# Kernel optimization log

Hardware: AMD Instinct MI355X
Metric: run time of the kernel (lower is better)

Reference implementation:

```python
import jax, jax.numpy as jnp
import numpy as np

EMB = 512
QKV = 512
H = 8      # num_heads
PH = 8     # num_pheads
HD = QKV // H
PHD = QKV // PH


def _make_params(key):
    names = ['Wi', 'Wip', 'Wic', 'Wq', 'Wpq', 'Wk', 'Wpk', 'Wv', 'Wpv', 'Wo', 'Wop']
    ks = jax.random.split(key, len(names))
    p = {}
    for n, k in zip(names, ks):
        din = EMB if n in ('Wi', 'Wip', 'Wic') else QKV
        dout = EMB if n in ('Wo', 'Wop') else QKV
        p[n] = jax.random.normal(k, (din, dout), jnp.float32) * 0.02
        p['b' + n[1:]] = jnp.zeros((dout,), jnp.float32)
    return p


def setup_inputs() -> dict:
    key = jax.random.key(0)
    kq, kp, kc, kw = jax.random.split(key, 4)
    B, S, P = 16, 4096, 64
    inp = {
        'query': jax.random.normal(kq, (B, S, EMB), jnp.float32),
        'pquery': jax.random.normal(kp, (B, P, EMB), jnp.float32),
        'context': jax.random.normal(kc, (B, S, EMB), jnp.float32),
    }
    inp.update(_make_params(kw))
    return inp


def reference(query, pquery, context,
              Wi, bi, Wip, bip, Wic, bic,
              Wq, bq, Wpq, bpq, Wk, bk, Wpk, bpk,
              Wv, bv, Wpv, bpv, Wo, bo, Wop, bop):
    # Dropout layers act as identity (eval mode / deterministic reference).
    B, S, _ = query.shape
    P = pquery.shape[1]

    q_in = query @ Wi + bi        # (B,S,QKV)
    pq_in = pquery @ Wip + bip    # (B,P,QKV)
    c_in = context @ Wic + bic    # (B,S,QKV)

    # --- pack stage: pquery attends over context -> p_context ---
    pq = ((pq_in @ Wpq + bpq) * (PHD ** -0.5)).reshape(B, P, PH, PHD)
    pk = (c_in @ Wpk + bpk).reshape(B, S, PH, PHD)
    pv = (c_in @ Wpv + bpv).reshape(B, S, PH, PHD)
    # dropout before softmax in original; identity here
    pattn = jax.nn.softmax(jnp.einsum('bphd,bshd->bhps', pq, pk), axis=-1)
    pc = jnp.einsum('bhps,bshd->bphd', pattn, pv).reshape(B, P, QKV)

    # --- unpack stage: query attends over p_context ---
    q = ((q_in @ Wq + bq) * (HD ** -0.5)).reshape(B, S, H, HD)
    k = (pc @ Wk + bk).reshape(B, P, H, HD)
    v = (pc @ Wv + bv).reshape(B, P, H, HD)
    aw = jax.nn.softmax(jnp.einsum('bshd,bphd->bhsp', q, k), axis=-1)  # (B,H,S,P)
    attn = jnp.einsum('bhsp,bphd->bshd', aw, v).reshape(B, S, QKV)
    attn = attn @ Wo + bo           # (B,S,EMB)
    pc_out = pc @ Wop + bop         # (B,P,EMB)

    # torch returns attn_weights as (S, B*H, P) when batch_first
    aw_t = jnp.transpose(aw.reshape(B * H, S, P), (1, 0, 2))
    return attn, pc_out, aw_t
```

## Files before the change

### kernel.cpp

```cpp
#include <hip/hip_runtime.h>


typedef __bf16 bf16x8 __attribute__((ext_vector_type(8)));
typedef float f32x4 __attribute__((ext_vector_type(4)));
typedef unsigned short u16x8 __attribute__((ext_vector_type(8)));
typedef unsigned short u16x4 __attribute__((ext_vector_type(4)));

#define MFMA16(a, b, c) __builtin_amdgcn_mfma_f32_16x16x32_bf16((a), (b), (c), 0, 0, 0)

__device__ __forceinline__ unsigned short f2bf_bits(float f) {
  unsigned int u = __float_as_uint(f);
  u += 0x7fffu + ((u >> 16) & 1u);
  return (unsigned short)(u >> 16);
}

__device__ __forceinline__ void gload16(const void* g, void* l) {
  __builtin_amdgcn_global_load_lds(
      (const __attribute__((address_space(1))) void*)g,
      (__attribute__((address_space(3))) void*)l, 16, 0, 0);
}

struct Ptr8 { const float* p[8]; };

__global__ __launch_bounds__(256) void prep_kernel(
    Ptr8 srcs, unsigned short* __restrict__ WT,
    const float* bi, const float* bip, const float* bic,
    const float* Wq, const float* Wpq, const float* Wpk, const float* Wpv,
    const float* bq, const float* bpq, const float* bpk, const float* bpv,
    float* __restrict__ bias_out) {
  const int t = threadIdx.x;
  if (blockIdx.z < 8) {
    const float* __restrict__ W = srcs.p[blockIdx.z];
    unsigned short* __restrict__ O = WT + (size_t)blockIdx.z * 262144;
    __shared__ float tile[32][33];
    const int tr = blockIdx.x * 32, tc = blockIdx.y * 32;
    {
      const int r = t >> 3, c4 = (t & 7) * 4;
      const float4 v = *reinterpret_cast<const float4*>(&W[(size_t)(tr + r) * 512 + tc + c4]);
      tile[r][c4 + 0] = v.x; tile[r][c4 + 1] = v.y; tile[r][c4 + 2] = v.z; tile[r][c4 + 3] = v.w;
    }
    __syncthreads();
    {
      const int n = t >> 3, k4 = (t & 7) * 4;
      u16x4 o;
#pragma unroll
      for (int j = 0; j < 4; j++) o[j] = f2bf_bits(tile[k4 + j][n]);
      *reinterpret_cast<u16x4*>(&O[(size_t)(tc + n) * 512 + tr + k4]) = o;
    }
  } else {
    const int idx = blockIdx.y * 16 + blockIdx.x;
    if (idx >= 8) return;
    const int y = idx >> 1;
    const float* bin  = (y == 0) ? bi : (y == 1) ? bip : bic;
    const float* W    = (y == 0) ? Wq : (y == 1) ? Wpq : (y == 2) ? Wpk : Wpv;
    const float* bout = (y == 0) ? bq : (y == 1) ? bpq : (y == 2) ? bpk : bpv;
    const float scale = (y < 2) ? 0.125f : 1.0f;
    const int n = (idx & 1) * 256 + t;
    float s = 0.f;
    for (int k = 0; k < 512; k++) s += bin[k] * W[(size_t)k * 512 + n];
    bias_out[y * 512 + n] = (s + bout[n]) * scale;
  }
}

__global__ __launch_bounds__(256) void gemm_wcomb(
    const float* __restrict__ Wi, const float* __restrict__ Wip,
    const float* __restrict__ Wic, const unsigned short* __restrict__ WTbase,
    unsigned short* __restrict__ outbase) {
  const int z = blockIdx.z;
  const float* __restrict__ A = (z == 0) ? Wi : (z == 1) ? Wip : Wic;
  const unsigned short* __restrict__ BT = WTbase + (size_t)z * 262144;
  unsigned short* __restrict__ out = outbase + (size_t)z * 262144;
  const float scale = (z < 2) ? 0.125f : 1.0f;

  __shared__ __align__(16) unsigned short As[128 * 72];
  __shared__ __align__(16) unsigned short Bs[128 * 72];
  const int t = threadIdx.x;
  const int w = t >> 6, l = t & 63, li = l & 15, lg = l >> 4;
  const int wm = w >> 1, wn = w & 1;
  const int m0 = blockIdx.x * 128, n0 = blockIdx.y * 128;

  f32x4 acc[4][4] = {};

  for (int kt = 0; kt < 512; kt += 64) {
#pragma unroll
    for (int i = 0; i < 8; i++) {
      const int row = i * 16 + (t >> 4), k = (t & 15) * 4;
      const float4 v = *reinterpret_cast<const float4*>(&A[(size_t)(m0 + row) * 512 + kt + k]);
      u16x4 o;
      o[0] = f2bf_bits(v.x); o[1] = f2bf_bits(v.y);
      o[2] = f2bf_bits(v.z); o[3] = f2bf_bits(v.w);
      *reinterpret_cast<u16x4*>(&As[row * 72 + k]) = o;
    }
#pragma unroll
    for (int i = 0; i < 4; i++) {
      const int row = i * 32 + (t >> 3), k = (t & 7) * 8;
      const u16x8 v = *reinterpret_cast<const u16x8*>(&BT[(size_t)(n0 + row) * 512 + kt + k]);
      *reinterpret_cast<u16x8*>(&Bs[row * 72 + k]) = v;
    }
    __syncthreads();
#pragma unroll
    for (int kk = 0; kk < 2; kk++) {
      bf16x8 a[4], b[4];
#pragma unroll
      for (int mf = 0; mf < 4; mf++)
        a[mf] = *reinterpret_cast<const bf16x8*>(&As[(wm * 64 + mf * 16 + li) * 72 + kk * 32 + lg * 8]);
#pragma unroll
      for (int nf = 0; nf < 4; nf++)
        b[nf] = *reinterpret_cast<const bf16x8*>(&Bs[(wn * 64 + nf * 16 + li) * 72 + kk * 32 + lg * 8]);
#pragma unroll
      for (int mf = 0; mf < 4; mf++)
#pragma unroll
        for (int nf = 0; nf < 4; nf++)
          acc[mf][nf] = MFMA16(a[mf], b[nf], acc[mf][nf]);
    }
    __syncthreads();
  }
  const int lg4 = lg * 4;
#pragma unroll
  for (int nf = 0; nf < 4; nf++) {
    const int col = n0 + wn * 64 + nf * 16 + li;
#pragma unroll
    for (int mf = 0; mf < 4; mf++) {
      const int row = m0 + wm * 64 + mf * 16 + lg4;
#pragma unroll
      for (int r = 0; r < 4; r++)
        out[(size_t)col * 512 + row + r] = f2bf_bits(acc[mf][nf][r] * scale);
    }
  }
}

template <typename AT, int OUTF32>
__device__ __forceinline__ void gemm2ph_body(
    const AT* __restrict__ A, const unsigned short* __restrict__ BT,
    const float* __restrict__ bias, void* out, int Ntiles, int ldc, int wg) {
  __shared__ __align__(16) unsigned short As[2][128 * 40];
  __shared__ __align__(16) unsigned short Bs[2][128 * 32];
  const int t = threadIdx.x;
  const int w = t >> 6, l = t & 63, li = l & 15, lg = l >> 4;
  const int wm = w >> 1, wn = w & 1;
  const int K = 512;
  const int m0 = (wg / Ntiles) * 128, n0 = (wg % Ntiles) * 128;

  f32x4 acc[4][4] = {};
  float4 aregf[4];
  u16x8 aregh[2];
  const int brow_ = t >> 2, bslot_ = t & 3;

#define ISSUE_A(kt)                                                            \
  if constexpr (sizeof(AT) == 4) {                                             \
    _Pragma("unroll") for (int i = 0; i < 4; i++)                              \
        aregf[i] = *reinterpret_cast<const float4*>(                           \
            &A[(size_t)(m0 + i * 32 + (t >> 3)) * K + (kt) + (t & 7) * 4]);    \
  } else {                                                                     \
    _Pragma("unroll") for (int i = 0; i < 2; i++)                              \
        aregh[i] = *reinterpret_cast<const u16x8*>(                            \
            &A[(size_t)(m0 + i * 64 + (t >> 2)) * K + (kt) + (t & 3) * 8]);    \
  }

#define WRITE_A(buf)                                                           \
  if constexpr (sizeof(AT) == 4) {                                             \
    _Pragma("unroll") for (int i = 0; i < 4; i++) {                            \
      const int row = i * 32 + (t >> 3);                                       \
      u16x4 o;                                                                 \
      o[0] = f2bf_bits(aregf[i].x); o[1] = f2bf_bits(aregf[i].y);              \
      o[2] = f2bf_bits(aregf[i].z); o[3] = f2bf_bits(aregf[i].w);              \
      *reinterpret_cast<u16x4*>(&As[buf][row * 40 + (t & 7) * 4]) = o;         \
    }                                                                          \
  } else {                                                                     \
    _Pragma("unroll") for (int i = 0; i < 2; i++) {                            \
      const int row = i * 64 + (t >> 2);                                       \
      *reinterpret_cast<u16x8*>(&As[buf][row * 40 + (t & 3) * 8]) = aregh[i];  \
    }                                                                          \
  }

#define STAGE_B(kt, buf)                                                       \
  {                                                                            \
    _Pragma("unroll") for (int i = 0; i < 2; i++) {                            \
      const int row = i * 64 + brow_;                                          \
      const int gs = (bslot_ ^ ((row >> 1) & 3)) * 8;                          \
      gload16(&BT[(size_t)(n0 + row) * K + (kt) + gs],                         \
              &Bs[buf][i * 2048 + t * 8]);                                     \
    }                                                                          \
  }

  ISSUE_A(0);
  STAGE_B(0, 0);
  WRITE_A(0);
  __syncthreads();

#pragma unroll 2
  for (int tt = 0; tt < 16; tt++) {
    const int cur = tt & 1, nxt = cur ^ 1;
    if (tt < 15) {
      STAGE_B((tt + 1) * 32, nxt);
      ISSUE_A((tt + 1) * 32);
    }
    bf16x8 a[4], b[4];
#pragma unroll
    for (int mf = 0; mf < 4; mf++) {
      const int r = wm * 64 + mf * 16 + li;
      a[mf] = *reinterpret_cast<const bf16x8*>(&As[cur][r * 40 + lg * 8]);
    }
#pragma unroll
    for (int nf = 0; nf < 4; nf++) {
      const int r = wn * 64 + nf * 16 + li;
      b[nf] = *reinterpret_cast<const bf16x8*>(
          &Bs[cur][r * 32 + ((lg ^ ((r >> 1) & 3)) * 8)]);
    }
#pragma unroll
    for (int mf = 0; mf < 4; mf++)
#pragma unroll
      for (int nf = 0; nf < 4; nf++)
        acc[mf][nf] = MFMA16(a[mf], b[nf], acc[mf][nf]);
    if (tt < 15) WRITE_A(nxt);
    __syncthreads();
  }
#undef ISSUE_A
#undef WRITE_A
#undef STAGE_B

  const int lg4 = lg * 4;
#pragma unroll
  for (int nf = 0; nf < 4; nf++) {
    const int col = n0 + wn * 64 + nf * 16 + li;
    const float bv = bias[col];
#pragma unroll
    for (int mf = 0; mf < 4; mf++) {
      const int row = m0 + wm * 64 + mf * 16 + lg4;
      if constexpr (OUTF32) {
        float* o = (float*)out;
#pragma unroll
        for (int r = 0; r < 4; r++)
          o[(size_t)(row + r) * ldc + col] = acc[mf][nf][r] + bv;
      } else {
        unsigned short* o = (unsigned short*)out;
#pragma unroll
        for (int r = 0; r < 4; r++)
          o[(size_t)(row + r) * ldc + col] = f2bf_bits(acc[mf][nf][r] + bv);
      }
    }
  }
}

__global__ __launch_bounds__(256, 4) void gemm2ph_qpkv(
    const float* query, const float* context, const float* pquery,
    const unsigned short* WqeT, const unsigned short* WpkveT,
    const unsigned short* WpqeT, const float* bqe, const float* bpkve,
    const float* bpqe, unsigned short* q_buf, unsigned short* pkv_buf,
    unsigned short* pq_buf) {
  const int q8 = gridDim.x >> 3;
  int wg = ((int)blockIdx.x & 7) * q8 + ((int)blockIdx.x >> 3);
  const float* A; const unsigned short* BT; const float* bias;
  unsigned short* out; int Ntiles, ldc;
  if (wg < 2048) {
    A = query; BT = WqeT; bias = bqe; out = q_buf; Ntiles = 4; ldc = 512;
  } else if (wg < 6144) {
    wg -= 2048; A = context; BT = WpkveT; bias = bpkve; out = pkv_buf;
    Ntiles = 8; ldc = 1024;
  } else {
    wg -= 6144; A = pquery; BT = WpqeT; bias = bpqe; out = pq_buf;
    Ntiles = 4; ldc = 512;
  }
  gemm2ph_body<float, 0>(A, BT, bias, out, Ntiles, ldc, wg);
}

__global__ __launch_bounds__(256, 4) void gemm2ph_final(
    const unsigned short* A, const unsigned short* BT, const float* bias,
    float* out) {
  const int q8 = gridDim.x >> 3;
  const int wg = ((int)blockIdx.x & 7) * q8 + ((int)blockIdx.x >> 3);
  gemm2ph_body<unsigned short, 1>(A, BT, bias, out, 4, 512, wg);
}

__global__ __launch_bounds__(256) void gemm_kvpc(
    const unsigned short* __restrict__ A, const unsigned short* __restrict__ BT,
    const float* __restrict__ bias0, const float* __restrict__ bias1,
    const float* __restrict__ bias2, unsigned short* out0, unsigned short* out1,
    float* out2, int Ntiles) {
  __shared__ __align__(16) unsigned short As[128 * 64];
  __shared__ __align__(16) unsigned short Bs[128 * 64];
  const int t = threadIdx.x;
  const int w = t >> 6, l = t & 63, li = l & 15, lg = l >> 4;
  const int wm = w >> 1, wn = w & 1;
  const int K = 512;
  const int m0 = (blockIdx.x / Ntiles) * 128, n0 = (blockIdx.x % Ntiles) * 128;

  f32x4 acc[4][4] = {};
  const int sr = t >> 3, sslot = t & 7;

  for (int kt = 0; kt < K; kt += 64) {
#pragma unroll
    for (int i = 0; i < 4; i++) {
      const int row = i * 32 + sr;
      const int gs = (sslot ^ (row & 7)) * 8;
      gload16(&A[(size_t)(m0 + row) * K + kt + gs], &As[(i * 256 + t) * 8]);
      gload16(&BT[(size_t)(n0 + row) * K + kt + gs], &Bs[(i * 256 + t) * 8]);
    }
    __syncthreads();
#pragma unroll
    for (int kk = 0; kk < 2; kk++) {
      bf16x8 a[4], b[4];
#pragma unroll
      for (int mf = 0; mf < 4; mf++) {
        const int r = wm * 64 + mf * 16 + li;
        a[mf] = *reinterpret_cast<const bf16x8*>(&As[r * 64 + (((kk * 4 + lg) ^ (r & 7)) * 8)]);
      }
#pragma unroll
      for (int nf = 0; nf < 4; nf++) {
        const int r = wn * 64 + nf * 16 + li;
        b[nf] = *reinterpret_cast<const bf16x8*>(&Bs[r * 64 + (((kk * 4 + lg) ^ (r & 7)) * 8)]);
      }
#pragma unroll
      for (int mf = 0; mf < 4; mf++)
#pragma unroll
        for (int nf = 0; nf < 4; nf++)
          acc[mf][nf] = MFMA16(a[mf], b[nf], acc[mf][nf]);
    }
    __syncthreads();
  }

  const int lg4 = lg * 4;
#pragma unroll
  for (int nf = 0; nf < 4; nf++) {
    const int col = n0 + wn * 64 + nf * 16 + li;
    if (col < 512) {
      const float bv = bias0[col];
#pragma unroll
      for (int mf = 0; mf < 4; mf++) {
        const int row = m0 + wm * 64 + mf * 16 + lg4;
#pragma unroll
        for (int r = 0; r < 4; r++)
          out0[(size_t)(row + r) * 512 + col] = f2bf_bits(acc[mf][nf][r] + bv);
      }
    } else if (col < 1024) {
      const float bv = bias1[col - 512];
#pragma unroll
      for (int mf = 0; mf < 4; mf++) {
        const int row = m0 + wm * 64 + mf * 16 + lg4;
#pragma unroll
        for (int r = 0; r < 4; r++)
          out1[(size_t)(row + r) * 512 + col - 512] = f2bf_bits(acc[mf][nf][r] + bv);
      }
    } else {
      const float bv = bias2[col - 1024];
#pragma unroll
      for (int mf = 0; mf < 4; mf++) {
        const int row = m0 + wm * 64 + mf * 16 + lg4;
#pragma unroll
        for (int r = 0; r < 4; r++)
          out2[(size_t)(row + r) * 512 + col - 1024] = acc[mf][nf][r] + bv;
      }
    }
  }
}

__global__ __launch_bounds__(256) void pack_attn(
    const unsigned short* __restrict__ pq_buf,
    const unsigned short* __restrict__ pkv_buf, float* __restrict__ partial) {
  __shared__ __align__(16) unsigned short pkL[64 * 72];
  __shared__ __align__(16) unsigned short pvT[64 * 72];
  __shared__ __align__(16) unsigned short prL[4 * 16 * 72];
  const int t = threadIdx.x, w = t >> 6, l = t & 63, li = l & 15, lg = l >> 4;
  const int bh = blockIdx.x, b = bh >> 3, h = bh & 7;
  const int sb = blockIdx.y * 512;

  bf16x8 aq[2];
  {
    const size_t base = ((size_t)(b * 64 + w * 16 + li)) * 512 + h * 64;
    aq[0] = *reinterpret_cast<const bf16x8*>(&pq_buf[base + lg * 8]);
    aq[1] = *reinterpret_cast<const bf16x8*>(&pq_buf[base + 32 + lg * 8]);
  }

  f32x4 acc[4] = {};
  float lsum[4] = {};

  for (int st = 0; st < 8; st++) {
    const int s0 = sb + st * 64;
#pragma unroll
    for (int i = 0; i < 2; i++) {
      const int row = i * 32 + (t >> 3), c = (t & 7) * 8;
      const u16x8 v = *reinterpret_cast<const u16x8*>(
          &pkv_buf[((size_t)(b * 4096 + s0 + row)) * 1024 + h * 64 + c]);
      *reinterpret_cast<u16x8*>(&pkL[row * 72 + c]) = v;
    }
    {
      const int rp = t >> 3, c = (t & 7) * 8;
      const size_t base = ((size_t)(b * 4096 + s0 + 2 * rp)) * 1024 + 512 + h * 64 + c;
      const u16x8 u0 = *reinterpret_cast<const u16x8*>(&pkv_buf[base]);
      const u16x8 u1 = *reinterpret_cast<const u16x8*>(&pkv_buf[base + 1024]);
#pragma unroll
      for (int j = 0; j < 8; j++) {
        const int val = ((int)u0[j] & 0xffff) | ((int)u1[j] << 16);
        *reinterpret_cast<int*>(&pvT[(c + j) * 72 + 2 * rp]) = val;
      }
    }
    __syncthreads();
    f32x4 sc[4] = {};
#pragma unroll
    for (int nf = 0; nf < 4; nf++) {
#pragma unroll
      for (int kk = 0; kk < 2; kk++) {
        const bf16x8 bk = *reinterpret_cast<const bf16x8*>(
            &pkL[(nf * 16 + li) * 72 + kk * 32 + lg * 8]);
        sc[nf] = MFMA16(aq[kk], bk, sc[nf]);
      }
    }
#pragma unroll
    for (int nf = 0; nf < 4; nf++) {
#pragma unroll
      for (int r = 0; r < 4; r++) {
        const float e = __expf(sc[nf][r]);
        lsum[r] += e;
        prL[(w * 16 + lg * 4 + r) * 72 + nf * 16 + li] = f2bf_bits(e);
      }
    }
#pragma unroll
    for (int kk = 0; kk < 2; kk++) {
      const bf16x8 ap = *reinterpret_cast<const bf16x8*>(
          &prL[(w * 16 + li) * 72 + kk * 32 + lg * 8]);
#pragma unroll
      for (int nf = 0; nf < 4; nf++) {
        const bf16x8 bv = *reinterpret_cast<const bf16x8*>(
            &pvT[(nf * 16 + li) * 72 + kk * 32 + lg * 8]);
        acc[nf] = MFMA16(ap, bv, acc[nf]);
      }
    }
    __syncthreads();
  }

#pragma unroll
  for (int m = 1; m < 16; m <<= 1)
#pragma unroll
    for (int r = 0; r < 4; r++) lsum[r] += __shfl_xor(lsum[r], m);

  const size_t pbase = ((size_t)(bh * 8 + blockIdx.y)) * 4160;
#pragma unroll
  for (int nf = 0; nf < 4; nf++)
#pragma unroll
    for (int r = 0; r < 4; r++)
      partial[pbase + (size_t)(w * 16 + lg * 4 + r) * 64 + nf * 16 + li] = acc[nf][r];
  if (li == 0)
#pragma unroll
    for (int r = 0; r < 4; r++) partial[pbase + 4096 + w * 16 + lg * 4 + r] = lsum[r];
}

__global__ __launch_bounds__(256) void pack_combine(const float* __restrict__ partial,
                                                    unsigned short* __restrict__ pc_buf) {
  const int bh = blockIdx.x, b = bh >> 3, h = bh & 7;
  const int t = threadIdx.x;
#pragma unroll
  for (int e = 0; e < 16; e++) {
    const int idx = e * 256 + t;
    const int p = idx >> 6, d = idx & 63;
    float s = 0.f, den = 0.f;
#pragma unroll
    for (int c = 0; c < 8; c++) {
      const float* pb = &partial[((size_t)(bh * 8 + c)) * 4160];
      s += pb[idx];
      den += pb[4096 + p];
    }
    pc_buf[((size_t)(b * 64 + p)) * 512 + h * 64 + d] = f2bf_bits(s / den);
  }
}

__global__ __launch_bounds__(256) void unpack_attn(
    const unsigned short* q_in, const unsigned short* __restrict__ k_buf,
    const unsigned short* __restrict__ v_buf, float* __restrict__ aw_out,
    unsigned short* attnh_out) {
  __shared__ __align__(16) unsigned short kL[64 * 72];
  __shared__ __align__(16) unsigned short vT[64 * 72];
  __shared__ __align__(16) unsigned short prL[4 * 64 * 72];
  const int t = threadIdx.x, w = t >> 6, l = t & 63, li = l & 15, lg = l >> 4;
  const int bh = blockIdx.y, b = bh >> 3, h = bh & 7;
  const int sbase = blockIdx.x * 256 + w * 64;

#pragma unroll
  for (int i = 0; i < 2; i++) {
    const int p = i * 32 + (t >> 3), c = (t & 7) * 8;
    const u16x8 v = *reinterpret_cast<const u16x8*>(
        &k_buf[((size_t)(b * 64 + p)) * 512 + h * 64 + c]);
    *reinterpret_cast<u16x8*>(&kL[p * 72 + c]) = v;
  }
  {
    const int rp = t >> 3, c = (t & 7) * 8;
    const size_t base = ((size_t)(b * 64 + 2 * rp)) * 512 + h * 64 + c;
    const u16x8 u0 = *reinterpret_cast<const u16x8*>(&v_buf[base]);
    const u16x8 u1 = *reinterpret_cast<const u16x8*>(&v_buf[base + 512]);
#pragma unroll
    for (int j = 0; j < 8; j++) {
      const int val = ((int)u0[j] & 0xffff) | ((int)u1[j] << 16);
      *reinterpret_cast<int*>(&vT[(c + j) * 72 + 2 * rp]) = val;
    }
  }
  bf16x8 aq[4][2];
#pragma unroll
  for (int mf = 0; mf < 4; mf++) {
    const size_t base = ((size_t)(b * 4096 + sbase + mf * 16 + li)) * 512 + h * 64;
    aq[mf][0] = *reinterpret_cast<const bf16x8*>(&q_in[base + lg * 8]);
    aq[mf][1] = *reinterpret_cast<const bf16x8*>(&q_in[base + 32 + lg * 8]);
  }
  __syncthreads();

  f32x4 sc[4][4] = {};
#pragma unroll
  for (int kk = 0; kk < 2; kk++)
#pragma unroll
    for (int nf = 0; nf < 4; nf++) {
      const bf16x8 bk = *reinterpret_cast<const bf16x8*>(
          &kL[(nf * 16 + li) * 72 + kk * 32 + lg * 8]);
#pragma unroll
      for (int mf = 0; mf < 4; mf++) sc[mf][nf] = MFMA16(aq[mf][kk], bk, sc[mf][nf]);
    }

#pragma unroll
  for (int mf = 0; mf < 4; mf++) {
#pragma unroll
    for (int r = 0; r < 4; r++) {
      float e[4];
      float rs = 0.f;
#pragma unroll
      for (int nf = 0; nf < 4; nf++) {
        e[nf] = __expf(sc[mf][nf][r]);
        rs += e[nf];
      }
#pragma unroll
      for (int m = 1; m < 16; m <<= 1) rs += __shfl_xor(rs, m);
      const float inv = 1.0f / rs;
      const int srow = sbase + mf * 16 + lg * 4 + r;
#pragma unroll
      for (int nf = 0; nf < 4; nf++) {
        const float pr = e[nf] * inv;
        aw_out[(size_t)srow * 8192 + bh * 64 + nf * 16 + li] = pr;
        prL[(w * 64 + mf * 16 + lg * 4 + r) * 72 + nf * 16 + li] = f2bf_bits(pr);
      }
    }
  }

  f32x4 acc[4][4] = {};
#pragma unroll
  for (int kk = 0; kk < 2; kk++)
#pragma unroll
    for (int mf = 0; mf < 4; mf++) {
      const bf16x8 ap = *reinterpret_cast<const bf16x8*>(
          &prL[(w * 64 + mf * 16 + li) * 72 + kk * 32 + lg * 8]);
#pragma unroll
      for (int nf = 0; nf < 4; nf++) {
        const bf16x8 bv = *reinterpret_cast<const bf16x8*>(
            &vT[(nf * 16 + li) * 72 + kk * 32 + lg * 8]);
        acc[mf][nf] = MFMA16(ap, bv, acc[mf][nf]);
      }
    }
#pragma unroll
  for (int mf = 0; mf < 4; mf++)
#pragma unroll
    for (int nf = 0; nf < 4; nf++)
#pragma unroll
      for (int r = 0; r < 4; r++)
        attnh_out[((size_t)(b * 4096 + sbase + mf * 16 + lg * 4 + r)) * 512 + h * 64 +
                  nf * 16 + li] = f2bf_bits(acc[mf][nf][r]);
}

extern "C" void kernel_launch(void* const* d_in, const int* in_sizes, int n_in,
                              void* d_out, int out_size, void* d_ws, size_t ws_size,
                              hipStream_t stream) {
  (void)in_sizes; (void)n_in; (void)out_size; (void)ws_size;

  const float* query   = (const float*)d_in[0];
  const float* pquery  = (const float*)d_in[1];
  const float* context = (const float*)d_in[2];
  const float* Wi  = (const float*)d_in[3];  const float* bi  = (const float*)d_in[4];
  const float* Wip = (const float*)d_in[5];  const float* bip = (const float*)d_in[6];
  const float* Wic = (const float*)d_in[7];  const float* bic = (const float*)d_in[8];
  const float* Wq  = (const float*)d_in[9];  const float* bq  = (const float*)d_in[10];
  const float* Wpq = (const float*)d_in[11]; const float* bpq = (const float*)d_in[12];
  const float* Wk  = (const float*)d_in[13]; const float* bk  = (const float*)d_in[14];
  const float* Wpk = (const float*)d_in[15]; const float* bpk = (const float*)d_in[16];
  const float* Wv  = (const float*)d_in[17]; const float* bv  = (const float*)d_in[18];
  const float* Wpv = (const float*)d_in[19]; const float* bpv = (const float*)d_in[20];
  const float* Wo  = (const float*)d_in[21]; const float* bo  = (const float*)d_in[22];
  const float* Wop = (const float*)d_in[23]; const float* bop = (const float*)d_in[24];

  char* ws = (char*)d_ws;
  unsigned short* WT     = (unsigned short*)(ws);
  unsigned short* WqeT   = (unsigned short*)(ws + 4u * 1024 * 1024);
  unsigned short* WpqeT  = WqeT + 512 * 512;
  unsigned short* WpkveT = WpqeT + 512 * 512;
  float* bqe   = (float*)(WpkveT + (size_t)1024 * 512);
  float* bpqe  = bqe + 512;
  float* bpkve = bpqe + 512;
  unsigned short* q_buf   = (unsigned short*)(ws + 8u * 1024 * 1024);
  unsigned short* pkv_buf = q_buf + (size_t)65536 * 512;
  unsigned short* pq_buf  = pkv_buf + (size_t)65536 * 1024;
  unsigned short* pc_buf  = pq_buf + (size_t)1024 * 512;
  unsigned short* k_buf   = pc_buf + (size_t)1024 * 512;
  unsigned short* v_buf   = k_buf + (size_t)1024 * 512;
  float* partial = (float*)(v_buf + (size_t)1024 * 512);

  float* out_attn = (float*)d_out;
  float* out_pc   = out_attn + (size_t)16 * 4096 * 512;
  float* out_aw   = out_pc + (size_t)16 * 64 * 512;

  const dim3 blk(256);

  Ptr8 tsrc; tsrc.p[0]=Wq; tsrc.p[1]=Wpq; tsrc.p[2]=Wpk; tsrc.p[3]=Wpv;
  tsrc.p[4]=Wk; tsrc.p[5]=Wv; tsrc.p[6]=Wop; tsrc.p[7]=Wo;
  prep_kernel<<<dim3(16, 16, 9), blk, 0, stream>>>(
      tsrc, WT, bi, bip, bic, Wq, Wpq, Wpk, Wpv, bq, bpq, bpk, bpv, bqe);
  gemm_wcomb<<<dim3(4, 4, 4), blk, 0, stream>>>(Wi, Wip, Wic, WT, WqeT);

  gemm2ph_qpkv<<<dim3(6176), blk, 0, stream>>>(
      query, context, pquery, WqeT, WpkveT, WpqeT, bqe, bpkve, bpqe,
      q_buf, pkv_buf, pq_buf);

  pack_attn<<<dim3(128, 8), blk, 0, stream>>>(pq_buf, pkv_buf, partial);
  pack_combine<<<128, blk, 0, stream>>>(partial, pc_buf);

  gemm_kvpc<<<dim3(96), blk, 0, stream>>>(
      pc_buf, WT + (size_t)4 * 262144, bk, bv, bop, k_buf, v_buf, out_pc, 12);

  unpack_attn<<<dim3(16, 128), blk, 0, stream>>>(q_buf, k_buf, v_buf, out_aw, q_buf);

  gemm2ph_final<<<dim3(2048), blk, 0, stream>>>(
      q_buf, WT + (size_t)7 * 262144, bo, out_attn);
}
```

Before: 504.8 us.

## Pre-convert fp32 inputs to bf16 and use 3-stage async LDS pipeline GEMM

Adds a separate conversion kernel that turns query, context and pquery into bf16 scratch copies held in the output buffers, so the projection GEMM can load both A and B tiles with direct global-to-LDS async loads. The GEMM body becomes a triple-buffered pipeline with explicit vmcnt waits and barriers instead of a register-staged double buffer that converted to bf16 on the fly. The cost is an extra pass that reads the fp32 inputs and writes bf16 copies, plus higher LDS use per block, with occupancy lowered to 3 blocks.

```diff
diff --git a/kernel.cpp b/kernel.cpp
--- a/kernel.cpp
+++ b/kernel.cpp
@@ -129,95 +129,113 @@
   }
 }
 
-template <typename AT, int OUTF32>
-__device__ __forceinline__ void gemm2ph_body(
-    const AT* __restrict__ A, const unsigned short* __restrict__ BT,
+__global__ __launch_bounds__(256) void conv_bf16(
+    const float* __restrict__ q, const float* __restrict__ c,
+    const float* __restrict__ pq, unsigned short* __restrict__ qo,
+    unsigned short* __restrict__ co, unsigned short* __restrict__ pqo) {
+  if (blockIdx.y == 2) {
+    if (blockIdx.x >= 256) return;
+    const size_t idx = (((size_t)blockIdx.x) * 256 + threadIdx.x) * 8;
+    const float4 v0 = *reinterpret_cast<const float4*>(&pq[idx]);
+    const float4 v1 = *reinterpret_cast<const float4*>(&pq[idx + 4]);
+    u16x8 o;
+    o[0] = f2bf_bits(v0.x); o[1] = f2bf_bits(v0.y); o[2] = f2bf_bits(v0.z); o[3] = f2bf_bits(v0.w);
+    o[4] = f2bf_bits(v1.x); o[5] = f2bf_bits(v1.y); o[6] = f2bf_bits(v1.z); o[7] = f2bf_bits(v1.w);
+    *reinterpret_cast<u16x8*>(&pqo[idx]) = o;
+    return;
+  }
+  const float* __restrict__ src = blockIdx.y ? c : q;
+  unsigned short* __restrict__ dst = blockIdx.y ? co : qo;
+#pragma unroll
+  for (int i = 0; i < 8; i++) {
+    const size_t idx = (((size_t)i * 2048 + blockIdx.x) * 256 + threadIdx.x) * 8;
+    const float4 v0 = *reinterpret_cast<const float4*>(&src[idx]);
+    const float4 v1 = *reinterpret_cast<const float4*>(&src[idx + 4]);
+    u16x8 o;
+    o[0] = f2bf_bits(v0.x); o[1] = f2bf_bits(v0.y); o[2] = f2bf_bits(v0.z); o[3] = f2bf_bits(v0.w);
+    o[4] = f2bf_bits(v1.x); o[5] = f2bf_bits(v1.y); o[6] = f2bf_bits(v1.z); o[7] = f2bf_bits(v1.w);
+    *reinterpret_cast<u16x8*>(&dst[idx]) = o;
+  }
+}
+
+#define WAITV(n)                                            \
+  {                                                         \
+    asm volatile("s_waitcnt vmcnt(" #n ")" ::: "memory");   \
+    __builtin_amdgcn_sched_barrier(0);                      \
+  }
+#define BAR3()                                              \
+  {                                                         \
+    __builtin_amdgcn_s_barrier();                           \
+    __builtin_amdgcn_sched_barrier(0);                      \
+  }
+
+template <int OUTF32>
+__device__ __forceinline__ void gemm3p_body(
+    const unsigned short* __restrict__ A, const unsigned short* __restrict__ BT,
     const float* __restrict__ bias, void* out, int Ntiles, int ldc, int wg) {
-  __shared__ __align__(16) unsigned short As[2][128 * 40];
-  __shared__ __align__(16) unsigned short Bs[2][128 * 32];
+  __shared__ __align__(16) unsigned short As[3][128 * 32];
+  __shared__ __align__(16) unsigned short Bs[3][128 * 32];
   const int t = threadIdx.x;
   const int w = t >> 6, l = t & 63, li = l & 15, lg = l >> 4;
   const int wm = w >> 1, wn = w & 1;
-  const int K = 512;
   const int m0 = (wg / Ntiles) * 128, n0 = (wg % Ntiles) * 128;
 
   f32x4 acc[4][4] = {};
-  float4 aregf[4];
-  u16x8 aregh[2];
-  const int brow_ = t >> 2, bslot_ = t & 3;
-
-#define ISSUE_A(kt)                                                            \
-  if constexpr (sizeof(AT) == 4) {                                             \
-    _Pragma("unroll") for (int i = 0; i < 4; i++)                              \
-        aregf[i] = *reinterpret_cast<const float4*>(                           \
-            &A[(size_t)(m0 + i * 32 + (t >> 3)) * K + (kt) + (t & 7) * 4]);    \
-  } else {                                                                     \
-    _Pragma("unroll") for (int i = 0; i < 2; i++)                              \
-        aregh[i] = *reinterpret_cast<const u16x8*>(                            \
-            &A[(size_t)(m0 + i * 64 + (t >> 2)) * K + (kt) + (t & 3) * 8]);    \
-  }
-
-#define WRITE_A(buf)                                                           \
-  if constexpr (sizeof(AT) == 4) {                                             \
-    _Pragma("unroll") for (int i = 0; i < 4; i++) {                            \
-      const int row = i * 32 + (t >> 3);                                       \
-      u16x4 o;                                                                 \
-      o[0] = f2bf_bits(aregf[i].x); o[1] = f2bf_bits(aregf[i].y);              \
-      o[2] = f2bf_bits(aregf[i].z); o[3] = f2bf_bits(aregf[i].w);              \
-      *reinterpret_cast<u16x4*>(&As[buf][row * 40 + (t & 7) * 4]) = o;         \
+  const int srow = t >> 2, sslot = t & 3;
+
+#define STAGE3(tile)                                                           \
+  {                                                                            \
+    const int bb = (tile) % 3;                                                 \
+    const int kt = (tile) * 32;                                                \
+    _Pragma("unroll") for (int i = 0; i < 2; i++) {                            \
+      const int row = i * 64 + srow;                                           \
+      const int gs = (sslot ^ ((row >> 1) & 3)) * 8;                           \
+      gload16(&A[(size_t)(m0 + row) * 512 + kt + gs], &As[bb][(i * 256 + t) * 8]); \
     }                                                                          \
-  } else {                                                                     \
     _Pragma("unroll") for (int i = 0; i < 2; i++) {                            \
-      const int row = i * 64 + (t >> 2);                                       \
-      *reinterpret_cast<u16x8*>(&As[buf][row * 40 + (t & 3) * 8]) = aregh[i];  \
+      const int row = i * 64 + srow;                                           \
+      const int gs = (sslot ^ ((row >> 1) & 3)) * 8;                           \
+      gload16(&BT[(size_t)(n0 + row) * 512 + kt + gs], &Bs[bb][(i * 256 + t) * 8]); \
     }                                                                          \
   }
 
-#define STAGE_B(kt, buf)                                                       \
+#define COMPUTE3(tile)                                                         \
   {                                                                            \
-    _Pragma("unroll") for (int i = 0; i < 2; i++) {                            \
-      const int row = i * 64 + brow_;                                          \
-      const int gs = (bslot_ ^ ((row >> 1) & 3)) * 8;                          \
-      gload16(&BT[(size_t)(n0 + row) * K + (kt) + gs],                         \
-              &Bs[buf][i * 2048 + t * 8]);                                     \
+    const int bb = (tile) % 3;                                                 \
+    bf16x8 a[4], b[4];                                                         \
+    _Pragma("unroll") for (int mf = 0; mf < 4; mf++) {                         \
+      const int r = wm * 64 + mf * 16 + li;                                    \
+      a[mf] = *reinterpret_cast<const bf16x8*>(                                \
+          &As[bb][r * 32 + ((lg ^ ((r >> 1) & 3)) * 8)]);                      \
     }                                                                          \
-  }
-
-  ISSUE_A(0);
-  STAGE_B(0, 0);
-  WRITE_A(0);
-  __syncthreads();
-
-#pragma unroll 2
-  for (int tt = 0; tt < 16; tt++) {
-    const int cur = tt & 1, nxt = cur ^ 1;
-    if (tt < 15) {
-      STAGE_B((tt + 1) * 32, nxt);
-      ISSUE_A((tt + 1) * 32);
-    }
-    bf16x8 a[4], b[4];
-#pragma unroll
-    for (int mf = 0; mf < 4; mf++) {
-      const int r = wm * 64 + mf * 16 + li;
-      a[mf] = *reinterpret_cast<const bf16x8*>(&As[cur][r * 40 + lg * 8]);
-    }
-#pragma unroll
-    for (int nf = 0; nf < 4; nf++) {
-      const int r = wn * 64 + nf * 16 + li;
-      b[nf] = *reinterpret_cast<const bf16x8*>(
-          &Bs[cur][r * 32 + ((lg ^ ((r >> 1) & 3)) * 8)]);
-    }
-#pragma unroll
-    for (int mf = 0; mf < 4; mf++)
-#pragma unroll
-      for (int nf = 0; nf < 4; nf++)
-        acc[mf][nf] = MFMA16(a[mf], b[nf], acc[mf][nf]);
-    if (tt < 15) WRITE_A(nxt);
-    __syncthreads();
-  }
-#undef ISSUE_A
-#undef WRITE_A
-#undef STAGE_B
+    _Pragma("unroll") for (int nf = 0; nf < 4; nf++) {                         \
+      const int r = wn * 64 + nf * 16 + li;                                    \
+      b[nf] = *reinterpret_cast<const bf16x8*>(                                \
+          &Bs[bb][r * 32 + ((lg ^ ((r >> 1) & 3)) * 8)]);                      \
+    }                                                                          \
+    _Pragma("unroll") for (int mf = 0; mf < 4; mf++)                           \
+        _Pragma("unroll") for (int nf = 0; nf < 4; nf++)                       \
+            acc[mf][nf] = MFMA16(a[mf], b[nf], acc[mf][nf]);                   \
+  }
+
+  STAGE3(0);
+  STAGE3(1);
+  STAGE3(2);
+
+#pragma unroll 1
+  for (int tt = 0; tt < 13; ++tt) {
+    WAITV(8);
+    BAR3();
+    COMPUTE3(tt);
+    BAR3();
+    STAGE3(tt + 3);
+  }
+  WAITV(8); BAR3(); COMPUTE3(13); BAR3();
+  WAITV(4); BAR3(); COMPUTE3(14); BAR3();
+  WAITV(0); BAR3(); COMPUTE3(15);
+
+#undef STAGE3
+#undef COMPUTE3
 
   const int lg4 = lg * 4;
 #pragma unroll
@@ -242,34 +260,37 @@
   }
 }
 
-__global__ __launch_bounds__(256, 4) void gemm2ph_qpkv(
-    const float* query, const float* context, const float* pquery,
-    const unsigned short* WqeT, const unsigned short* WpkveT,
-    const unsigned short* WpqeT, const float* bqe, const float* bpkve,
-    const float* bpqe, unsigned short* q_buf, unsigned short* pkv_buf,
-    unsigned short* pq_buf) {
+__global__ __launch_bounds__(256, 3) void gemm3p_qpkv(
+    const unsigned short* q_bf, const unsigned short* c_bf,
+    const unsigned short* pq_bf, const unsigned short* WqeT,
+    const unsigned short* WpkveT, const unsigned short* WpqeT,
+    const float* bqe, const float* bpkve, const float* bpqe,
+    unsigned short* q_buf, unsigned short* pkv_buf, unsigned short* pq_buf) {
   const int q8 = gridDim.x >> 3;
   int wg = ((int)blockIdx.x & 7) * q8 + ((int)blockIdx.x >> 3);
-  const float* A; const unsigned short* BT; const float* bias;
-  unsigned short* out; int Ntiles, ldc;
+  const unsigned short* A;
+  const unsigned short* BT;
+  const float* bias;
+  unsigned short* out;
+  int Ntiles, ldc;
   if (wg < 2048) {
-    A = query; BT = WqeT; bias = bqe; out = q_buf; Ntiles = 4; ldc = 512;
+    A = q_bf; BT = WqeT; bias = bqe; out = q_buf; Ntiles = 4; ldc = 512;
   } else if (wg < 6144) {
-    wg -= 2048; A = context; BT = WpkveT; bias = bpkve; out = pkv_buf;
+    wg -= 2048; A = c_bf; BT = WpkveT; bias = bpkve; out = pkv_buf;
     Ntiles = 8; ldc = 1024;
   } else {
-    wg -= 6144; A = pquery; BT = WpqeT; bias = bpqe; out = pq_buf;
+    wg -= 6144; A = pq_bf; BT = WpqeT; bias = bpqe; out = pq_buf;
     Ntiles = 4; ldc = 512;
   }
-  gemm2ph_body<float, 0>(A, BT, bias, out, Ntiles, ldc, wg);
-}
-
-__global__ __launch_bounds__(256, 4) void gemm2ph_final(
+  gemm3p_body<0>(A, BT, bias, out, Ntiles, ldc, wg);
+}
+
+__global__ __launch_bounds__(256, 3) void gemm3p_final(
     const unsigned short* A, const unsigned short* BT, const float* bias,
     float* out) {
   const int q8 = gridDim.x >> 3;
   const int wg = ((int)blockIdx.x & 7) * q8 + ((int)blockIdx.x >> 3);
-  gemm2ph_body<unsigned short, 1>(A, BT, bias, out, 4, 512, wg);
+  gemm3p_body<1>(A, BT, bias, out, 4, 512, wg);
 }
 
 __global__ __launch_bounds__(256) void gemm_kvpc(
@@ -588,6 +609,7 @@
   float* bqe   = (float*)(WpkveT + (size_t)1024 * 512);
   float* bpqe  = bqe + 512;
   float* bpkve = bpqe + 512;
+  unsigned short* pq_bf = (unsigned short*)(ws + 7u * 1024 * 1024);
   unsigned short* q_buf   = (unsigned short*)(ws + 8u * 1024 * 1024);
   unsigned short* pkv_buf = q_buf + (size_t)65536 * 512;
   unsigned short* pq_buf  = pkv_buf + (size_t)65536 * 1024;
@@ -600,6 +622,9 @@
   float* out_pc   = out_attn + (size_t)16 * 4096 * 512;
   float* out_aw   = out_pc + (size_t)16 * 64 * 512;
 
+  unsigned short* c_bf = (unsigned short*)out_attn;
+  unsigned short* q_bf = (unsigned short*)out_aw;
+
   const dim3 blk(256);
 
   Ptr8 tsrc; tsrc.p[0]=Wq; tsrc.p[1]=Wpq; tsrc.p[2]=Wpk; tsrc.p[3]=Wpv;
@@ -608,8 +633,11 @@
       tsrc, WT, bi, bip, bic, Wq, Wpq, Wpk, Wpv, bq, bpq, bpk, bpv, bqe);
   gemm_wcomb<<<dim3(4, 4, 4), blk, 0, stream>>>(Wi, Wip, Wic, WT, WqeT);
 
-  gemm2ph_qpkv<<<dim3(6176), blk, 0, stream>>>(
-      query, context, pquery, WqeT, WpkveT, WpqeT, bqe, bpkve, bpqe,
+  conv_bf16<<<dim3(2048, 3), blk, 0, stream>>>(query, context, pquery,
+                                               q_bf, c_bf, pq_bf);
+
+  gemm3p_qpkv<<<dim3(6176), blk, 0, stream>>>(
+      q_bf, c_bf, pq_bf, WqeT, WpkveT, WpqeT, bqe, bpkve, bpqe,
       q_buf, pkv_buf, pq_buf);
 
   pack_attn<<<dim3(128, 8), blk, 0, stream>>>(pq_buf, pkv_buf, partial);
@@ -620,6 +648,6 @@
 
   unpack_attn<<<dim3(16, 128), blk, 0, stream>>>(q_buf, k_buf, v_buf, out_aw, q_buf);
 
-  gemm2ph_final<<<dim3(2048), blk, 0, stream>>>(
+  gemm3p_final<<<dim3(2048), blk, 0, stream>>>(
       q_buf, WT + (size_t)7 * 262144, bo, out_attn);
 }
```

New measurement: 532.3 us. 1.05x slower.

## Load A fragments directly to registers and triple-buffer B in GEMMs

Applied to the files above, without the earlier changes.

The main projection GEMMs stop staging the A operand through shared memory. Each wave now loads its own MFMA A fragments straight from global memory into registers and converts fp32 to bf16 in registers. The B tiles move to a 3-stage LDS ring with explicit vmcnt waits and raw barriers, so loads run further ahead of compute. This removes LDS writes and reads for A. The cost is redundant global A loads across the two wn waves, higher register pressure, and occupancy lowered from 4 to 3 blocks per CU.

```diff
diff --git a/kernel.cpp b/kernel.cpp
--- a/kernel.cpp
+++ b/kernel.cpp
@@ -129,95 +129,112 @@
   }
 }
 
-template <typename AT, int OUTF32>
-__device__ __forceinline__ void gemm2ph_body(
-    const AT* __restrict__ A, const unsigned short* __restrict__ BT,
+#define WAITV(n)                                            \
+  {                                                         \
+    asm volatile("s_waitcnt vmcnt(" #n ")" ::: "memory");   \
+    __builtin_amdgcn_sched_barrier(0);                      \
+  }
+#define BAR3()                                              \
+  {                                                         \
+    __builtin_amdgcn_s_barrier();                           \
+    __builtin_amdgcn_sched_barrier(0);                      \
+  }
+
+template <int AF32, int OUTF32>
+__device__ __forceinline__ void gemm_areg_body(
+    const void* __restrict__ Av, const unsigned short* __restrict__ BT,
     const float* __restrict__ bias, void* out, int Ntiles, int ldc, int wg) {
-  __shared__ __align__(16) unsigned short As[2][128 * 40];
-  __shared__ __align__(16) unsigned short Bs[2][128 * 32];
+  __shared__ __align__(16) unsigned short Bs[3][128 * 32];
   const int t = threadIdx.x;
   const int w = t >> 6, l = t & 63, li = l & 15, lg = l >> 4;
   const int wm = w >> 1, wn = w & 1;
-  const int K = 512;
   const int m0 = (wg / Ntiles) * 128, n0 = (wg % Ntiles) * 128;
 
   f32x4 acc[4][4] = {};
-  float4 aregf[4];
-  u16x8 aregh[2];
+  float4 rawA[4][2];
+  u16x8 rawH[4];
+  bf16x8 af[4];
   const int brow_ = t >> 2, bslot_ = t & 3;
 
-#define ISSUE_A(kt)                                                            \
-  if constexpr (sizeof(AT) == 4) {                                             \
-    _Pragma("unroll") for (int i = 0; i < 4; i++)                              \
-        aregf[i] = *reinterpret_cast<const float4*>(                           \
-            &A[(size_t)(m0 + i * 32 + (t >> 3)) * K + (kt) + (t & 7) * 4]);    \
-  } else {                                                                     \
-    _Pragma("unroll") for (int i = 0; i < 2; i++)                              \
-        aregh[i] = *reinterpret_cast<const u16x8*>(                            \
-            &A[(size_t)(m0 + i * 64 + (t >> 2)) * K + (kt) + (t & 3) * 8]);    \
-  }
-
-#define WRITE_A(buf)                                                           \
-  if constexpr (sizeof(AT) == 4) {                                             \
-    _Pragma("unroll") for (int i = 0; i < 4; i++) {                            \
-      const int row = i * 32 + (t >> 3);                                       \
-      u16x4 o;                                                                 \
-      o[0] = f2bf_bits(aregf[i].x); o[1] = f2bf_bits(aregf[i].y);              \
-      o[2] = f2bf_bits(aregf[i].z); o[3] = f2bf_bits(aregf[i].w);              \
-      *reinterpret_cast<u16x4*>(&As[buf][row * 40 + (t & 7) * 4]) = o;         \
-    }                                                                          \
-  } else {                                                                     \
-    _Pragma("unroll") for (int i = 0; i < 2; i++) {                            \
-      const int row = i * 64 + (t >> 2);                                       \
-      *reinterpret_cast<u16x8*>(&As[buf][row * 40 + (t & 3) * 8]) = aregh[i];  \
-    }                                                                          \
-  }
-
-#define STAGE_B(kt, buf)                                                       \
+  const float* apf = (const float*)Av + (size_t)(m0 + wm * 64 + li) * 512 + lg * 8;
+  const unsigned short* aph =
+      (const unsigned short*)Av + (size_t)(m0 + wm * 64 + li) * 512 + lg * 8;
+
+#define STAGE_B(tile)                                                          \
   {                                                                            \
+    const int bb = (tile) % 3;                                                 \
+    const int kt = (tile) * 32;                                                \
     _Pragma("unroll") for (int i = 0; i < 2; i++) {                            \
       const int row = i * 64 + brow_;                                          \
       const int gs = (bslot_ ^ ((row >> 1) & 3)) * 8;                          \
-      gload16(&BT[(size_t)(n0 + row) * K + (kt) + gs],                         \
-              &Bs[buf][i * 2048 + t * 8]);                                     \
+      gload16(&BT[(size_t)(n0 + row) * 512 + kt + gs],                         \
+              &Bs[bb][(i * 256 + t) * 8]);                                     \
     }                                                                          \
   }
 
+#define ISSUE_A(kt)                                                            \
+  if constexpr (AF32) {                                                        \
+    _Pragma("unroll") for (int mf = 0; mf < 4; mf++) {                         \
+      rawA[mf][0] = *reinterpret_cast<const float4*>(apf + (size_t)mf * 8192 + (kt)); \
+      rawA[mf][1] = *reinterpret_cast<const float4*>(apf + (size_t)mf * 8192 + (kt) + 4); \
+    }                                                                          \
+  } else {                                                                     \
+    _Pragma("unroll") for (int mf = 0; mf < 4; mf++)                           \
+        rawH[mf] = *reinterpret_cast<const u16x8*>(aph + (size_t)mf * 8192 + (kt)); \
+  }
+
+#define CVT_A()                                                                \
+  if constexpr (AF32) {                                                        \
+    _Pragma("unroll") for (int mf = 0; mf < 4; mf++) {                         \
+      bf16x8 v;                                                                \
+      _Pragma("unroll") for (int j = 0; j < 4; j++) {                          \
+        v[j] = (__bf16)rawA[mf][0][j];                                         \
+        v[j + 4] = (__bf16)rawA[mf][1][j];                                     \
+      }                                                                        \
+      af[mf] = v;                                                              \
+    }                                                                          \
+  } else {                                                                     \
+    _Pragma("unroll") for (int mf = 0; mf < 4; mf++)                           \
+        af[mf] = *reinterpret_cast<const bf16x8*>(&rawH[mf]);                  \
+  }
+
+#define COMPUTE(tile)                                                          \
+  {                                                                            \
+    const int bb = (tile) % 3;                                                 \
+    bf16x8 bfr[4];                                                             \
+    _Pragma("unroll") for (int nf = 0; nf < 4; nf++) {                         \
+      const int r = wn * 64 + nf * 16 + li;                                    \
+      bfr[nf] = *reinterpret_cast<const bf16x8*>(                              \
+          &Bs[bb][r * 32 + ((lg ^ ((r >> 1) & 3)) * 8)]);                      \
+    }                                                                          \
+    _Pragma("unroll") for (int mf = 0; mf < 4; mf++)                           \
+        _Pragma("unroll") for (int nf = 0; nf < 4; nf++)                       \
+            acc[mf][nf] = MFMA16(af[mf], bfr[nf], acc[mf][nf]);                \
+  }
+
   ISSUE_A(0);
-  STAGE_B(0, 0);
-  WRITE_A(0);
-  __syncthreads();
-
-#pragma unroll 2
-  for (int tt = 0; tt < 16; tt++) {
-    const int cur = tt & 1, nxt = cur ^ 1;
-    if (tt < 15) {
-      STAGE_B((tt + 1) * 32, nxt);
-      ISSUE_A((tt + 1) * 32);
-    }
-    bf16x8 a[4], b[4];
-#pragma unroll
-    for (int mf = 0; mf < 4; mf++) {
-      const int r = wm * 64 + mf * 16 + li;
-      a[mf] = *reinterpret_cast<const bf16x8*>(&As[cur][r * 40 + lg * 8]);
-    }
-#pragma unroll
-    for (int nf = 0; nf < 4; nf++) {
-      const int r = wn * 64 + nf * 16 + li;
-      b[nf] = *reinterpret_cast<const bf16x8*>(
-          &Bs[cur][r * 32 + ((lg ^ ((r >> 1) & 3)) * 8)]);
-    }
-#pragma unroll
-    for (int mf = 0; mf < 4; mf++)
-#pragma unroll
-      for (int nf = 0; nf < 4; nf++)
-        acc[mf][nf] = MFMA16(a[mf], b[nf], acc[mf][nf]);
-    if (tt < 15) WRITE_A(nxt);
-    __syncthreads();
-  }
+  STAGE_B(0);
+  STAGE_B(1);
+
+#pragma unroll 1
+  for (int tt = 0; tt < 15; ++tt) {
+    WAITV(2);
+    CVT_A();
+    ISSUE_A((tt + 1) * 32);
+    if (tt < 14) STAGE_B(tt + 2);
+    BAR3();
+    COMPUTE(tt);
+    BAR3();
+  }
+  WAITV(0);
+  CVT_A();
+  BAR3();
+  COMPUTE(15);
+
+#undef STAGE_B
 #undef ISSUE_A
-#undef WRITE_A
-#undef STAGE_B
+#undef CVT_A
+#undef COMPUTE
 
   const int lg4 = lg * 4;
 #pragma unroll
@@ -242,7 +259,7 @@
   }
 }
 
-__global__ __launch_bounds__(256, 4) void gemm2ph_qpkv(
+__global__ __launch_bounds__(256, 3) void gemm_areg_qpkv(
     const float* query, const float* context, const float* pquery,
     const unsigned short* WqeT, const unsigned short* WpkveT,
     const unsigned short* WpqeT, const float* bqe, const float* bpkve,
@@ -250,8 +267,11 @@
     unsigned short* pq_buf) {
   const int q8 = gridDim.x >> 3;
   int wg = ((int)blockIdx.x & 7) * q8 + ((int)blockIdx.x >> 3);
-  const float* A; const unsigned short* BT; const float* bias;
-  unsigned short* out; int Ntiles, ldc;
+  const float* A;
+  const unsigned short* BT;
+  const float* bias;
+  unsigned short* out;
+  int Ntiles, ldc;
   if (wg < 2048) {
     A = query; BT = WqeT; bias = bqe; out = q_buf; Ntiles = 4; ldc = 512;
   } else if (wg < 6144) {
@@ -261,15 +281,15 @@
     wg -= 6144; A = pquery; BT = WpqeT; bias = bpqe; out = pq_buf;
     Ntiles = 4; ldc = 512;
   }
-  gemm2ph_body<float, 0>(A, BT, bias, out, Ntiles, ldc, wg);
-}
-
-__global__ __launch_bounds__(256, 4) void gemm2ph_final(
+  gemm_areg_body<1, 0>(A, BT, bias, out, Ntiles, ldc, wg);
+}
+
+__global__ __launch_bounds__(256, 3) void gemm_areg_final(
     const unsigned short* A, const unsigned short* BT, const float* bias,
     float* out) {
   const int q8 = gridDim.x >> 3;
   const int wg = ((int)blockIdx.x & 7) * q8 + ((int)blockIdx.x >> 3);
-  gemm2ph_body<unsigned short, 1>(A, BT, bias, out, 4, 512, wg);
+  gemm_areg_body<0, 1>(A, BT, bias, out, 4, 512, wg);
 }
 
 __global__ __launch_bounds__(256) void gemm_kvpc(
@@ -608,7 +628,7 @@
       tsrc, WT, bi, bip, bic, Wq, Wpq, Wpk, Wpv, bq, bpq, bpk, bpv, bqe);
   gemm_wcomb<<<dim3(4, 4, 4), blk, 0, stream>>>(Wi, Wip, Wic, WT, WqeT);
 
-  gemm2ph_qpkv<<<dim3(6176), blk, 0, stream>>>(
+  gemm_areg_qpkv<<<dim3(6176), blk, 0, stream>>>(
       query, context, pquery, WqeT, WpkveT, WpqeT, bqe, bpkve, bpqe,
       q_buf, pkv_buf, pq_buf);
 
@@ -620,6 +640,6 @@
 
   unpack_attn<<<dim3(16, 128), blk, 0, stream>>>(q_buf, k_buf, v_buf, out_aw, q_buf);
 
-  gemm2ph_final<<<dim3(2048), blk, 0, stream>>>(
+  gemm_areg_final<<<dim3(2048), blk, 0, stream>>>(
       q_buf, WT + (size_t)7 * 262144, bo, out_attn);
 }
```

Result: slower. 781.5 us (+54.8%).
